# Kernel tuning notes

Hardware: AMD Instinct MI355X
Metric: run time of the kernel (lower is better)

The kernel has to match this reference:

```python
import jax, jax.numpy as jnp
import numpy as np

C = 256          # channels
H = 8            # attn_heads
B = 2048         # number of graphs
NPG = 128        # nodes per graph
N = B * NPG      # total nodes
EPS = 1e-5


def setup_inputs() -> dict:
    key = jax.random.key(0)
    ks = jax.random.split(key, 16)
    s = 1.0 / np.sqrt(C)
    seg = jnp.repeat(jnp.arange(B, dtype=jnp.int32), NPG)          # sorted, all segments present
    batch = jnp.stack([seg, seg], axis=1)                           # [N, 2]; column 0 = graph id
    return {
        "x": jax.random.normal(ks[0], (N, C), dtype=jnp.float32),
        "batch": batch,
        "num_graphs": B,
        "W1": jax.random.normal(ks[1], (C, C), dtype=jnp.float32) * s,
        "b1": jnp.zeros((C,), jnp.float32),
        "gamma": jnp.ones((C,), jnp.float32),
        "beta": jnp.zeros((C,), jnp.float32),
        "W2": jax.random.normal(ks[2], (C, C), dtype=jnp.float32) * s,
        "b2": jnp.zeros((C,), jnp.float32),
        "Wq": jax.random.normal(ks[3], (C, C), dtype=jnp.float32) * s,
        "bq": jnp.zeros((C,), jnp.float32),
        "Wk": jax.random.normal(ks[4], (C, C), dtype=jnp.float32) * s,
        "bk": jnp.zeros((C,), jnp.float32),
        "Wv": jax.random.normal(ks[5], (C, C), dtype=jnp.float32) * s,
        "bv": jnp.zeros((C,), jnp.float32),
        "Wo": jax.random.normal(ks[6], (C, C), dtype=jnp.float32) * s,
        "bo": jnp.zeros((C,), jnp.float32),
        "Wr": jax.random.normal(ks[7], (1, C), dtype=jnp.float32) * s,
        "br": jnp.zeros((1,), jnp.float32),
    }


def reference(x, batch, num_graphs, W1, b1, gamma, beta, W2, b2,
              Wq, bq, Wk, bk, Wv, bv, Wo, bo, Wr, br):
    seg = batch[:, 0]                                   # [N] graph ids, sorted
    Dh = C // H
    scale = 1.0 / np.sqrt(Dh)

    # trunk: Linear -> BatchNorm1d (train-mode batch stats) -> ReLU -> Linear
    h = x @ W1.T + b1                                   # [N, C]
    mu = h.mean(axis=0)
    var = h.var(axis=0)                                 # biased, as torch uses for normalization
    h = (h - mu) * jax.lax.rsqrt(var + EPS) * gamma + beta
    h = jax.nn.relu(h)
    h = h @ W2.T + b2                                   # [N, C]

    # single-query MHA pooled per graph segment (query = ones(C))
    q = jnp.ones((C,), h.dtype)
    qh = (q @ Wq.T + bq).reshape(H, Dh)                 # [H, Dh] shared across graphs
    kh = (h @ Wk.T + bk).reshape(N, H, Dh)              # [N, H, Dh]
    vh = (h @ Wv.T + bv).reshape(N, H, Dh)

    logits = jnp.einsum('nhd,hd->nh', kh, qh) * scale   # [N, H]
    # segment softmax over each graph's nodes
    m = jax.ops.segment_max(logits, seg, num_segments=num_graphs)   # [B, H]
    p = jnp.exp(logits - m[seg])                                     # [N, H]
    denom = jax.ops.segment_sum(p, seg, num_segments=num_graphs)     # [B, H]
    attn = p / denom[seg]                                            # [N, H]

    pooled = jax.ops.segment_sum(attn[:, :, None] * vh, seg,
                                 num_segments=num_graphs)            # [B, H, Dh]
    pooled = pooled.reshape(num_graphs, C) @ Wo.T + bo               # out_proj -> [B, C]

    out = jnp.tanh(pooled @ Wr.T + br)                               # [B, 1]
    return out
```

## Files before the change

### kernel.cpp

```cpp
#include <hip/hip_runtime.h>
#include <hip/hip_bf16.h>
#include <math.h>

#define C_DIM 256
#define H_HEADS 8
#define B_GRAPHS 2048
#define NPG 128
#define N_NODES (B_GRAPHS * NPG)
#define EPS 1e-5f
#define SCALE_ATT 0.17677669529663687f

typedef short bf16x8 __attribute__((ext_vector_type(8)));
typedef float f32x4 __attribute__((ext_vector_type(4)));

__device__ __forceinline__ unsigned short f2bf(float f) {
    __hip_bfloat16 h = __float2bfloat16(f);
    union { __hip_bfloat16 h; unsigned short u; } cv; cv.h = h; return cv.u;
}
__device__ __forceinline__ float bf2f(unsigned short u) {
    union { unsigned int i; float f; } v; v.i = ((unsigned int)u) << 16; return v.f;
}


__global__ __launch_bounds__(256) void prep1_kernel(
    const float* __restrict__ Wq, const float* __restrict__ bq,
    const float* __restrict__ Wk, const float* __restrict__ bk,
    const float* __restrict__ Wo, const float* __restrict__ Wr,
    float* __restrict__ wk_eff, float* __restrict__ lbias, float* __restrict__ wor)
{
    __shared__ float qhS[256];
    __shared__ float WrS[256];
    const int t = threadIdx.x;
    {
        float s = bq[t];
        const float* row = Wq + (size_t)t * 256;
        for (int c = 0; c < 256; c += 4) {
            float4 v = *(const float4*)&row[c];
            s += v.x + v.y + v.z + v.w;
        }
        qhS[t] = s;
        WrS[t] = Wr[t];
    }
    __syncthreads();
    for (int it = 0; it < 8; ++it) {
        int idx = t + it * 256;
        int head = idx >> 8, c = idx & 255;
        float acc = 0.f;
        #pragma unroll 4
        for (int d = 0; d < 32; ++d)
            acc = fmaf(Wk[(size_t)(head * 32 + d) * 256 + c], qhS[head * 32 + d], acc);
        wk_eff[head * 256 + c] = acc * SCALE_ATT;
    }
    if (t < 8) {
        float acc = 0.f;
        for (int d = 0; d < 32; ++d) acc = fmaf(bk[t * 32 + d], qhS[t * 32 + d], acc);
        lbias[t] = acc * SCALE_ATT;
    }
    {
        float acc = 0.f;
        for (int j2 = 0; j2 < 256; ++j2)
            acc = fmaf(Wo[(size_t)j2 * 256 + t], WrS[j2], acc);
        wor[t] = acc;
    }
}

__global__ __launch_bounds__(256) void prep2_kernel(
    const float* __restrict__ W2, const float* __restrict__ b2,
    const float* __restrict__ Wv, const float* __restrict__ wk_eff,
    const float* __restrict__ lbias, const float* __restrict__ wor_g,
    float* __restrict__ wfT, float* __restrict__ bfold, float* __restrict__ V_g)
{
    __shared__ float wkS[256];
    const int t = threadIdx.x, head = blockIdx.x;
    wkS[t] = wk_eff[head * 256 + t];
    __syncthreads();
    float acc = 0.f;
    #pragma unroll 4
    for (int cp = 0; cp < 256; ++cp)
        acc = fmaf(W2[(size_t)cp * 256 + t], wkS[cp], acc);
    wfT[head * 256 + t] = acc;
    float accv = 0.f;
    #pragma unroll 4
    for (int d = 0; d < 32; ++d) {
        int j = head * 32 + d;
        accv = fmaf(Wv[(size_t)j * 256 + t], wor_g[j], accv);
    }
    V_g[head * 256 + t] = accv;
    if (t == 0) {
        float b = lbias[head];
        for (int cp = 0; cp < 256; ++cp) b = fmaf(b2[cp], wkS[cp], b);
        bfold[head] = b;
    }
}

__global__ __launch_bounds__(256) void prep3_kernel(
    const float* __restrict__ W2, const float* __restrict__ V_g, float* __restrict__ G_g)
{
    __shared__ float vS[256];
    const int t = threadIdx.x, head = blockIdx.x;
    vS[t] = V_g[head * 256 + t];
    __syncthreads();
    float acc = 0.f;
    #pragma unroll 4
    for (int cp = 0; cp < 256; ++cp)
        acc = fmaf(W2[(size_t)cp * 256 + t], vS[cp], acc);
    G_g[t * 8 + head] = acc;
}

__global__ __launch_bounds__(256) void prep4_kernel(
    const float* __restrict__ b2, const float* __restrict__ bv,
    const float* __restrict__ bo, const float* __restrict__ Wr,
    const float* __restrict__ br, const float* __restrict__ V_g,
    const float* __restrict__ wor, float* __restrict__ c0)
{
    __shared__ float red[256];
    const int t = threadIdx.x;
    float vs = 0.f;
    #pragma unroll
    for (int h = 0; h < 8; ++h) vs += V_g[h * 256 + t];
    red[t] = b2[t] * vs + bv[t] * wor[t] + bo[t] * Wr[t];
    __syncthreads();
    for (int s = 128; s > 0; s >>= 1) {
        if (t < s) red[t] += red[t + s];
        __syncthreads();
    }
    if (t == 0) c0[0] = red[0] + br[0];
}

__global__ __launch_bounds__(256) void w1cvt_kernel(
    const float* __restrict__ W1, unsigned short* __restrict__ W1bf)
{
    int i = blockIdx.x * 256 + threadIdx.x;
    W1bf[i] = f2bf(W1[i]);
}

__global__ __launch_bounds__(256) void gemm1_kernel(
    const float* __restrict__ x, const unsigned short* __restrict__ W1bf,
    unsigned short* __restrict__ h1bf,
    float* __restrict__ parts1, float* __restrict__ parts2)
{
    __shared__ unsigned short Alds[128 * 40];
    __shared__ unsigned short Blds[256 * 40];
    const int t = threadIdx.x;
    const int lane = t & 63, w = t >> 6;
    const int l15 = lane & 15, kg = lane >> 4;
    const size_t n0 = (size_t)blockIdx.x * 128;

    f32x4 acc[2][16];
    #pragma unroll
    for (int mt = 0; mt < 2; ++mt)
        #pragma unroll
        for (int nt = 0; nt < 16; ++nt)
            acc[mt][nt] = (f32x4){0.f, 0.f, 0.f, 0.f};

    for (int kk = 0; kk < 8; ++kk) {
        if (kk) __syncthreads();
        #pragma unroll
        for (int p = 0; p < 4; ++p) {
            int i = p * 256 + t;
            {
                int row = i >> 3, kq = i & 7;
                float4 v = *(const float4*)&x[(n0 + row) * 256 + kk * 32 + kq * 4];
                ushort4 u;
                u.x = f2bf(v.x); u.y = f2bf(v.y); u.z = f2bf(v.z); u.w = f2bf(v.w);
                *(ushort4*)&Alds[row * 40 + kq * 4] = u;
            }
            {
                int row = i >> 2, seg = i & 3;
                bf16x8 bv = *(const bf16x8*)&W1bf[(size_t)row * 256 + kk * 32 + seg * 8];
                *(bf16x8*)&Blds[row * 40 + seg * 8] = bv;
            }
        }
        __syncthreads();
        bf16x8 a0 = *(const bf16x8*)&Alds[(w * 32 + l15) * 40 + kg * 8];
        bf16x8 a1 = *(const bf16x8*)&Alds[(w * 32 + 16 + l15) * 40 + kg * 8];
        #pragma unroll
        for (int nt = 0; nt < 16; ++nt) {
            bf16x8 b = *(const bf16x8*)&Blds[(nt * 16 + l15) * 40 + kg * 8];
            acc[0][nt] = __builtin_amdgcn_mfma_f32_16x16x32_bf16(a0, b, acc[0][nt], 0, 0, 0);
            acc[1][nt] = __builtin_amdgcn_mfma_f32_16x16x32_bf16(a1, b, acc[1][nt], 0, 0, 0);
        }
    }

    float s1[16], s2[16];
    #pragma unroll
    for (int nt = 0; nt < 16; ++nt) { s1[nt] = 0.f; s2[nt] = 0.f; }
    #pragma unroll
    for (int mt = 0; mt < 2; ++mt)
        #pragma unroll
        for (int nt = 0; nt < 16; ++nt)
            #pragma unroll
            for (int r = 0; r < 4; ++r) {
                float f = acc[mt][nt][r];
                size_t row = n0 + w * 32 + mt * 16 + kg * 4 + r;
                h1bf[row * 256 + nt * 16 + l15] = f2bf(f);
                s1[nt] += f;
                s2[nt] += f * f;
            }
    #pragma unroll
    for (int nt = 0; nt < 16; ++nt) {
        s1[nt] += __shfl_xor(s1[nt], 16);
        s1[nt] += __shfl_xor(s1[nt], 32);
        s2[nt] += __shfl_xor(s2[nt], 16);
        s2[nt] += __shfl_xor(s2[nt], 32);
    }
    if (lane < 16) {
        size_t prow = ((size_t)blockIdx.x * 4 + w) * 256;
        #pragma unroll
        for (int nt = 0; nt < 16; ++nt) {
            parts1[prow + nt * 16 + lane] = s1[nt];
            parts2[prow + nt * 16 + lane] = s2[nt];
        }
    }
}

__global__ __launch_bounds__(256) void reduce_kernel(
    const float* __restrict__ P1, const float* __restrict__ P2,
    float* __restrict__ psum, float* __restrict__ psum2)
{
    const int t = threadIdx.x;
    const int b = blockIdx.x;
    float s = 0.f, s2 = 0.f;
    for (int r = 0; r < 128; ++r) {
        size_t row = (size_t)(b * 128 + r) * 256;
        s += P1[row + t];
        s2 += P2[row + t];
    }
    atomicAdd(&psum[t], s);
    atomicAdd(&psum2[t], s2);
}

__global__ __launch_bounds__(256) void stats_kernel(
    const float* __restrict__ psum, const float* __restrict__ psum2,
    const float* __restrict__ gamma, const float* __restrict__ beta,
    float* __restrict__ sc, float* __restrict__ sh)
{
    const int t = threadIdx.x;
    const float invN = 1.0f / (float)N_NODES;
    float S = psum[t], S2 = psum2[t];
    float mu = S * invN;
    float var = S2 * invN - mu * mu;
    float rstd = rsqrtf(var + EPS);
    float g = gamma[t] * rstd;
    sc[t] = g;
    sh[t] = beta[t] - mu * g;
}

__global__ __launch_bounds__(256, 2) void fused_kernel(
    const unsigned short* __restrict__ h1bf, const float* __restrict__ sc_g,
    const float* __restrict__ sh_g, const float* __restrict__ wfT_g,
    const float* __restrict__ bfold, const float* __restrict__ G_g,
    const float* __restrict__ c0_g, float* __restrict__ out)
{
    __shared__ __align__(16) float S[13220];
    float* scS     = S;
    float* shS     = S + 256;
    float* wfTS    = S + 512;
    float* logitsS = S + 2560;
    float* attnS   = S + 3616;
    float* AtS     = S + 4640;
    float* redP    = S + 6688;
    float* redS    = S + 8992;
    unsigned short* aSu = (unsigned short*)(S + 8996);

    const int t = threadIdx.x;
    const int g = blockIdx.x;

    scS[t] = sc_g[t];
    shS[t] = sh_g[t];
    #pragma unroll
    for (int q = 0; q < 8; ++q) wfTS[t + q * 256] = wfT_g[t + q * 256];

    const int n_dot = t & 31, ce = t >> 5;
    const int h_red = t >> 5, n_red = t & 31;

    for (int chunk = 0; chunk < 4; ++chunk) {
        __syncthreads();
        #pragma unroll
        for (int p = 0; p < 4; ++p) {
            int i = p * 256 + t;
            int row = i >> 5, seg = i & 31;
            const bf16x8 hv = *(const bf16x8*)&h1bf[((size_t)(g * 128 + chunk * 32 + row)) * 256 + seg * 8];
            float4 sc0 = *(const float4*)&scS[seg * 8];
            float4 sc1 = *(const float4*)&scS[seg * 8 + 4];
            float4 sh0 = *(const float4*)&shS[seg * 8];
            float4 sh1 = *(const float4*)&shS[seg * 8 + 4];
            bf16x8 av;
            av[0] = (short)f2bf(fmaxf(fmaf(bf2f((unsigned short)hv[0]), sc0.x, sh0.x), 0.f));
            av[1] = (short)f2bf(fmaxf(fmaf(bf2f((unsigned short)hv[1]), sc0.y, sh0.y), 0.f));
            av[2] = (short)f2bf(fmaxf(fmaf(bf2f((unsigned short)hv[2]), sc0.z, sh0.z), 0.f));
            av[3] = (short)f2bf(fmaxf(fmaf(bf2f((unsigned short)hv[3]), sc0.w, sh0.w), 0.f));
            av[4] = (short)f2bf(fmaxf(fmaf(bf2f((unsigned short)hv[4]), sc1.x, sh1.x), 0.f));
            av[5] = (short)f2bf(fmaxf(fmaf(bf2f((unsigned short)hv[5]), sc1.y, sh1.y), 0.f));
            av[6] = (short)f2bf(fmaxf(fmaf(bf2f((unsigned short)hv[6]), sc1.z, sh1.z), 0.f));
            av[7] = (short)f2bf(fmaxf(fmaf(bf2f((unsigned short)hv[7]), sc1.w, sh1.w), 0.f));
            *(bf16x8*)&aSu[row * 264 + seg * 8] = av;
        }
        __syncthreads();
        {
            float lacc[8];
            #pragma unroll
            for (int h = 0; h < 8; ++h) lacc[h] = 0.f;
            #pragma unroll
            for (int i = 0; i < 4; ++i) {
                const bf16x8 a8 = *(const bf16x8*)&aSu[n_dot * 264 + ce * 32 + i * 8];
                float af[8];
                #pragma unroll
                for (int j = 0; j < 8; ++j) af[j] = bf2f((unsigned short)a8[j]);
                #pragma unroll
                for (int h = 0; h < 8; ++h) {
                    const float4 w0 = *(const float4*)&wfTS[h * 256 + ce * 32 + i * 8];
                    const float4 w1 = *(const float4*)&wfTS[h * 256 + ce * 32 + i * 8 + 4];
                    lacc[h] = fmaf(af[0], w0.x, fmaf(af[1], w0.y, fmaf(af[2], w0.z, fmaf(af[3], w0.w,
                              fmaf(af[4], w1.x, fmaf(af[5], w1.y, fmaf(af[6], w1.z, fmaf(af[7], w1.w, lacc[h]))))))));
                }
            }
            #pragma unroll
            for (int h = 0; h < 8; ++h) redP[(ce * 32 + n_dot) * 9 + h] = lacc[h];
        }
        __syncthreads();
        {
            float L = bfold[h_red];
            #pragma unroll
            for (int ce2 = 0; ce2 < 8; ++ce2) L += redP[(ce2 * 32 + n_red) * 9 + h_red];
            logitsS[h_red * 132 + chunk * 32 + n_red] = L;
        }
    }
    __syncthreads();

    {
        const int head = t >> 5, j = t & 31;
        float l0 = logitsS[head * 132 + j];
        float l1 = logitsS[head * 132 + j + 32];
        float l2 = logitsS[head * 132 + j + 64];
        float l3 = logitsS[head * 132 + j + 96];
        float m = fmaxf(fmaxf(l0, l1), fmaxf(l2, l3));
        for (int s = 16; s > 0; s >>= 1) m = fmaxf(m, __shfl_xor(m, s, 32));
        float p0 = expf(l0 - m), p1 = expf(l1 - m), p2 = expf(l2 - m), p3 = expf(l3 - m);
        float sum = p0 + p1 + p2 + p3;
        for (int s = 16; s > 0; s >>= 1) sum += __shfl_xor(sum, s, 32);
        float inv = 1.0f / sum;
        attnS[(j + 0) * 8 + head] = p0 * inv;
        attnS[(j + 32) * 8 + head] = p1 * inv;
        attnS[(j + 64) * 8 + head] = p2 * inv;
        attnS[(j + 96) * 8 + head] = p3 * inv;
    }
    __syncthreads();

    {
        float acc[8];
        #pragma unroll
        for (int h = 0; h < 8; ++h) acc[h] = 0.f;
        const float scv = scS[t], shv = shS[t];
        const unsigned short* hp = h1bf + (size_t)g * 128 * 256 + t;
        #pragma unroll 4
        for (int n = 0; n < 128; ++n) {
            float hv = bf2f(hp[n * 256]);
            float a = fmaxf(fmaf(hv, scv, shv), 0.f);
            const float4 w0 = *(const float4*)&attnS[n * 8];
            const float4 w1 = *(const float4*)&attnS[n * 8 + 4];
            acc[0] = fmaf(a, w0.x, acc[0]);
            acc[1] = fmaf(a, w0.y, acc[1]);
            acc[2] = fmaf(a, w0.z, acc[2]);
            acc[3] = fmaf(a, w0.w, acc[3]);
            acc[4] = fmaf(a, w1.x, acc[4]);
            acc[5] = fmaf(a, w1.y, acc[5]);
            acc[6] = fmaf(a, w1.z, acc[6]);
            acc[7] = fmaf(a, w1.w, acc[7]);
        }
        #pragma unroll
        for (int h = 0; h < 8; ++h) AtS[t * 8 + h] = acc[h];
    }
    __syncthreads();

    {
        float4 a0 = *(const float4*)&AtS[t * 8];
        float4 a1 = *(const float4*)&AtS[t * 8 + 4];
        float4 g0 = *(const float4*)&G_g[t * 8];
        float4 g1 = *(const float4*)&G_g[t * 8 + 4];
        float term = a0.x * g0.x + a0.y * g0.y + a0.z * g0.z + a0.w * g0.w +
                     a1.x * g1.x + a1.y * g1.y + a1.z * g1.z + a1.w * g1.w;
        for (int s = 32; s > 0; s >>= 1) term += __shfl_xor(term, s);
        if ((t & 63) == 0) redS[t >> 6] = term;
        __syncthreads();
        if (t == 0) out[g] = tanhf(redS[0] + redS[1] + redS[2] + redS[3] + c0_g[0]);
    }
}

#define FOFF_WKE 0
#define FOFF_LB  2048
#define FOFF_WFT 2064
#define FOFF_BFD 4112
#define FOFF_WOR 4128
#define FOFF_V   4384
#define FOFF_G   6432
#define FOFF_C0  8480
#define FOFF_PS  8484
#define FOFF_PS2 8740
#define FOFF_SC  8996
#define FOFF_SH  9252
#define FOFF_P1  9512
#define FOFF_P2  (9512 + 2097152)

extern "C" void kernel_launch(void* const* d_in, const int* in_sizes, int n_in,
                              void* d_out, int out_size, void* d_ws, size_t ws_size,
                              hipStream_t stream)
{
    (void)in_sizes; (void)n_in; (void)out_size; (void)ws_size;
    const float* x     = (const float*)d_in[0];
    const float* W1    = (const float*)d_in[3];
    const float* gamma = (const float*)d_in[5];
    const float* beta  = (const float*)d_in[6];
    const float* W2    = (const float*)d_in[7];
    const float* b2    = (const float*)d_in[8];
    const float* Wq    = (const float*)d_in[9];
    const float* bq    = (const float*)d_in[10];
    const float* Wk    = (const float*)d_in[11];
    const float* bk    = (const float*)d_in[12];
    const float* Wv    = (const float*)d_in[13];
    const float* bv    = (const float*)d_in[14];
    const float* Wo    = (const float*)d_in[15];
    const float* bo    = (const float*)d_in[16];
    const float* Wr    = (const float*)d_in[17];
    const float* br    = (const float*)d_in[18];

    unsigned short* h1bf = (unsigned short*)d_ws;
    unsigned short* W1bf = h1bf + (size_t)N_NODES * 256;
    float* fbase = (float*)(W1bf + 65536);

    float* wk_eff = fbase + FOFF_WKE;
    float* lbias  = fbase + FOFF_LB;
    float* wfT    = fbase + FOFF_WFT;
    float* bfold  = fbase + FOFF_BFD;
    float* wor    = fbase + FOFF_WOR;
    float* V_g    = fbase + FOFF_V;
    float* G_g    = fbase + FOFF_G;
    float* c0     = fbase + FOFF_C0;
    float* psum   = fbase + FOFF_PS;
    float* psum2  = fbase + FOFF_PS2;
    float* sc     = fbase + FOFF_SC;
    float* sh     = fbase + FOFF_SH;
    float* P1     = fbase + FOFF_P1;
    float* P2     = fbase + FOFF_P2;

    hipMemsetAsync((void*)psum, 0, 512 * sizeof(float), stream);

    hipLaunchKernelGGL(prep1_kernel, dim3(1), dim3(256), 0, stream,
                       Wq, bq, Wk, bk, Wo, Wr, wk_eff, lbias, wor);
    hipLaunchKernelGGL(w1cvt_kernel, dim3(256), dim3(256), 0, stream, W1, W1bf);
    hipLaunchKernelGGL(prep2_kernel, dim3(8), dim3(256), 0, stream,
                       W2, b2, Wv, wk_eff, lbias, wor, wfT, bfold, V_g);
    hipLaunchKernelGGL(prep3_kernel, dim3(8), dim3(256), 0, stream, W2, V_g, G_g);
    hipLaunchKernelGGL(prep4_kernel, dim3(1), dim3(256), 0, stream,
                       b2, bv, bo, Wr, br, V_g, wor, c0);
    hipLaunchKernelGGL(gemm1_kernel, dim3(N_NODES / 128), dim3(256), 0, stream,
                       x, W1bf, h1bf, P1, P2);
    hipLaunchKernelGGL(reduce_kernel, dim3(64), dim3(256), 0, stream, P1, P2, psum, psum2);
    hipLaunchKernelGGL(stats_kernel, dim3(1), dim3(256), 0, stream,
                       psum, psum2, gamma, beta, sc, sh);
    hipLaunchKernelGGL(fused_kernel, dim3(B_GRAPHS), dim3(256), 0, stream,
                       h1bf, sc, sh, wfT, bfold, G_g, c0, (float*)d_out);
}
```

Measured before the change: 647.0 us.

## Compute per-graph logits and value projections with MFMA over a repacked h1 layout

```diff
diff --git a/kernel.cpp b/kernel.cpp
--- a/kernel.cpp
+++ b/kernel.cpp
@@ -9,6 +9,7 @@
 #define N_NODES (B_GRAPHS * NPG)
 #define EPS 1e-5f
 #define SCALE_ATT 0.17677669529663687f
+#define AST 264
 
 typedef short bf16x8 __attribute__((ext_vector_type(8)));
 typedef float f32x4 __attribute__((ext_vector_type(4)));
@@ -24,9 +25,9 @@
 
 __global__ __launch_bounds__(256) void prep1_kernel(
     const float* __restrict__ Wq, const float* __restrict__ bq,
-    const float* __restrict__ Wk, const float* __restrict__ bk,
+    const float* __restrict__ Wk,
     const float* __restrict__ Wo, const float* __restrict__ Wr,
-    float* __restrict__ wk_eff, float* __restrict__ lbias, float* __restrict__ wor)
+    float* __restrict__ wk_eff, float* __restrict__ wor)
 {
     __shared__ float qhS[256];
     __shared__ float WrS[256];
@@ -51,11 +52,6 @@
             acc = fmaf(Wk[(size_t)(head * 32 + d) * 256 + c], qhS[head * 32 + d], acc);
         wk_eff[head * 256 + c] = acc * SCALE_ATT;
     }
-    if (t < 8) {
-        float acc = 0.f;
-        for (int d = 0; d < 32; ++d) acc = fmaf(bk[t * 32 + d], qhS[t * 32 + d], acc);
-        lbias[t] = acc * SCALE_ATT;
-    }
     {
         float acc = 0.f;
         for (int j2 = 0; j2 < 256; ++j2)
@@ -65,10 +61,9 @@
 }
 
 __global__ __launch_bounds__(256) void prep2_kernel(
-    const float* __restrict__ W2, const float* __restrict__ b2,
-    const float* __restrict__ Wv, const float* __restrict__ wk_eff,
-    const float* __restrict__ lbias, const float* __restrict__ wor_g,
-    float* __restrict__ wfT, float* __restrict__ bfold, float* __restrict__ V_g)
+    const float* __restrict__ W2, const float* __restrict__ Wv,
+    const float* __restrict__ wk_eff, const float* __restrict__ wor_g,
+    unsigned short* __restrict__ WBg, float* __restrict__ V_g)
 {
     __shared__ float wkS[256];
     const int t = threadIdx.x, head = blockIdx.x;
@@ -78,7 +73,7 @@
     #pragma unroll 4
     for (int cp = 0; cp < 256; ++cp)
         acc = fmaf(W2[(size_t)cp * 256 + t], wkS[cp], acc);
-    wfT[head * 256 + t] = acc;
+    WBg[head * 256 + t] = f2bf(acc);
     float accv = 0.f;
     #pragma unroll 4
     for (int d = 0; d < 32; ++d) {
@@ -86,15 +81,11 @@
         accv = fmaf(Wv[(size_t)j * 256 + t], wor_g[j], accv);
     }
     V_g[head * 256 + t] = accv;
-    if (t == 0) {
-        float b = lbias[head];
-        for (int cp = 0; cp < 256; ++cp) b = fmaf(b2[cp], wkS[cp], b);
-        bfold[head] = b;
-    }
 }
 
 __global__ __launch_bounds__(256) void prep3_kernel(
-    const float* __restrict__ W2, const float* __restrict__ V_g, float* __restrict__ G_g)
+    const float* __restrict__ W2, const float* __restrict__ V_g,
+    unsigned short* __restrict__ WBg)
 {
     __shared__ float vS[256];
     const int t = threadIdx.x, head = blockIdx.x;
@@ -104,7 +95,7 @@
     #pragma unroll 4
     for (int cp = 0; cp < 256; ++cp)
         acc = fmaf(W2[(size_t)cp * 256 + t], vS[cp], acc);
-    G_g[t * 8 + head] = acc;
+    WBg[(8 + head) * 256 + t] = f2bf(acc);
 }
 
 __global__ __launch_bounds__(256) void prep4_kernel(
@@ -136,7 +127,7 @@
 
 __global__ __launch_bounds__(256) void gemm1_kernel(
     const float* __restrict__ x, const unsigned short* __restrict__ W1bf,
-    unsigned short* __restrict__ h1bf,
+    unsigned short* __restrict__ h1s,
     float* __restrict__ parts1, float* __restrict__ parts2)
 {
     __shared__ unsigned short Alds[128 * 40];
@@ -185,18 +176,19 @@
     float s1[16], s2[16];
     #pragma unroll
     for (int nt = 0; nt < 16; ++nt) { s1[nt] = 0.f; s2[nt] = 0.f; }
+    const size_t rowqBase = (n0 >> 2) + (size_t)w * 8;
     #pragma unroll
     for (int mt = 0; mt < 2; ++mt)
         #pragma unroll
-        for (int nt = 0; nt < 16; ++nt)
-            #pragma unroll
-            for (int r = 0; r < 4; ++r) {
-                float f = acc[mt][nt][r];
-                size_t row = n0 + w * 32 + mt * 16 + kg * 4 + r;
-                h1bf[row * 256 + nt * 16 + l15] = f2bf(f);
-                s1[nt] += f;
-                s2[nt] += f * f;
-            }
+        for (int nt = 0; nt < 16; ++nt) {
+            float f0 = acc[mt][nt][0], f1 = acc[mt][nt][1];
+            float f2v = acc[mt][nt][2], f3 = acc[mt][nt][3];
+            s1[nt] += (f0 + f1) + (f2v + f3);
+            s2[nt] += (f0 * f0 + f1 * f1) + (f2v * f2v + f3 * f3);
+            ushort4 u;
+            u.x = f2bf(f0); u.y = f2bf(f1); u.z = f2bf(f2v); u.w = f2bf(f3);
+            *(ushort4*)&h1s[(rowqBase + mt * 4 + kg) * 1024 + (nt * 16 + l15) * 4] = u;
+        }
     #pragma unroll
     for (int nt = 0; nt < 16; ++nt) {
         s1[nt] += __shfl_xor(s1[nt], 16);
@@ -246,161 +238,116 @@
     sh[t] = beta[t] - mu * g;
 }
 
-__global__ __launch_bounds__(256, 2) void fused_kernel(
-    const unsigned short* __restrict__ h1bf, const float* __restrict__ sc_g,
-    const float* __restrict__ sh_g, const float* __restrict__ wfT_g,
-    const float* __restrict__ bfold, const float* __restrict__ G_g,
+__global__ __launch_bounds__(256, 1) void fused_kernel(
+    const unsigned short* __restrict__ h1s, const float* __restrict__ sc_g,
+    const float* __restrict__ sh_g, const unsigned short* __restrict__ WBg,
     const float* __restrict__ c0_g, float* __restrict__ out)
 {
-    __shared__ __align__(16) float S[13220];
-    float* scS     = S;
-    float* shS     = S + 256;
-    float* wfTS    = S + 512;
-    float* logitsS = S + 2560;
-    float* attnS   = S + 3616;
-    float* AtS     = S + 4640;
-    float* redP    = S + 6688;
-    float* redS    = S + 8992;
-    unsigned short* aSu = (unsigned short*)(S + 8996);
+    __shared__ __align__(16) unsigned short aS[128 * AST];
+    __shared__ __align__(16) unsigned short WBl[16 * AST];
+    __shared__ float scS[256], shS[256];
+    __shared__ float LG[128 * 17];
+    __shared__ float redH[8];
+    __shared__ float c0S;
 
     const int t = threadIdx.x;
     const int g = blockIdx.x;
+    const int lane = t & 63, w = t >> 6;
+    const int l15 = lane & 15, kg = lane >> 4;
 
     scS[t] = sc_g[t];
     shS[t] = sh_g[t];
-    #pragma unroll
-    for (int q = 0; q < 8; ++q) wfTS[t + q * 256] = wfT_g[t + q * 256];
-
-    const int n_dot = t & 31, ce = t >> 5;
-    const int h_red = t >> 5, n_red = t & 31;
-
-    for (int chunk = 0; chunk < 4; ++chunk) {
-        __syncthreads();
-        #pragma unroll
-        for (int p = 0; p < 4; ++p) {
-            int i = p * 256 + t;
-            int row = i >> 5, seg = i & 31;
-            const bf16x8 hv = *(const bf16x8*)&h1bf[((size_t)(g * 128 + chunk * 32 + row)) * 256 + seg * 8];
-            float4 sc0 = *(const float4*)&scS[seg * 8];
-            float4 sc1 = *(const float4*)&scS[seg * 8 + 4];
-            float4 sh0 = *(const float4*)&shS[seg * 8];
-            float4 sh1 = *(const float4*)&shS[seg * 8 + 4];
-            bf16x8 av;
-            av[0] = (short)f2bf(fmaxf(fmaf(bf2f((unsigned short)hv[0]), sc0.x, sh0.x), 0.f));
-            av[1] = (short)f2bf(fmaxf(fmaf(bf2f((unsigned short)hv[1]), sc0.y, sh0.y), 0.f));
-            av[2] = (short)f2bf(fmaxf(fmaf(bf2f((unsigned short)hv[2]), sc0.z, sh0.z), 0.f));
-            av[3] = (short)f2bf(fmaxf(fmaf(bf2f((unsigned short)hv[3]), sc0.w, sh0.w), 0.f));
-            av[4] = (short)f2bf(fmaxf(fmaf(bf2f((unsigned short)hv[4]), sc1.x, sh1.x), 0.f));
-            av[5] = (short)f2bf(fmaxf(fmaf(bf2f((unsigned short)hv[5]), sc1.y, sh1.y), 0.f));
-            av[6] = (short)f2bf(fmaxf(fmaf(bf2f((unsigned short)hv[6]), sc1.z, sh1.z), 0.f));
-            av[7] = (short)f2bf(fmaxf(fmaf(bf2f((unsigned short)hv[7]), sc1.w, sh1.w), 0.f));
-            *(bf16x8*)&aSu[row * 264 + seg * 8] = av;
-        }
-        __syncthreads();
-        {
-            float lacc[8];
-            #pragma unroll
-            for (int h = 0; h < 8; ++h) lacc[h] = 0.f;
-            #pragma unroll
-            for (int i = 0; i < 4; ++i) {
-                const bf16x8 a8 = *(const bf16x8*)&aSu[n_dot * 264 + ce * 32 + i * 8];
-                float af[8];
-                #pragma unroll
-                for (int j = 0; j < 8; ++j) af[j] = bf2f((unsigned short)a8[j]);
-                #pragma unroll
-                for (int h = 0; h < 8; ++h) {
-                    const float4 w0 = *(const float4*)&wfTS[h * 256 + ce * 32 + i * 8];
-                    const float4 w1 = *(const float4*)&wfTS[h * 256 + ce * 32 + i * 8 + 4];
-                    lacc[h] = fmaf(af[0], w0.x, fmaf(af[1], w0.y, fmaf(af[2], w0.z, fmaf(af[3], w0.w,
-                              fmaf(af[4], w1.x, fmaf(af[5], w1.y, fmaf(af[6], w1.z, fmaf(af[7], w1.w, lacc[h]))))))));
-                }
-            }
-            #pragma unroll
-            for (int h = 0; h < 8; ++h) redP[(ce * 32 + n_dot) * 9 + h] = lacc[h];
-        }
-        __syncthreads();
-        {
-            float L = bfold[h_red];
-            #pragma unroll
-            for (int ce2 = 0; ce2 < 8; ++ce2) L += redP[(ce2 * 32 + n_red) * 9 + h_red];
-            logitsS[h_red * 132 + chunk * 32 + n_red] = L;
-        }
-    }
-    __syncthreads();
-
     {
-        const int head = t >> 5, j = t & 31;
-        float l0 = logitsS[head * 132 + j];
-        float l1 = logitsS[head * 132 + j + 32];
-        float l2 = logitsS[head * 132 + j + 64];
-        float l3 = logitsS[head * 132 + j + 96];
-        float m = fmaxf(fmaxf(l0, l1), fmaxf(l2, l3));
+        int j = t >> 4, cc = (t & 15) * 16;
+        bf16x8 w0 = *(const bf16x8*)&WBg[j * 256 + cc];
+        bf16x8 w1 = *(const bf16x8*)&WBg[j * 256 + cc + 8];
+        *(bf16x8*)&WBl[j * AST + cc] = w0;
+        *(bf16x8*)&WBl[j * AST + cc + 8] = w1;
+    }
+    if (t == 0) c0S = c0_g[0];
+    __syncthreads();
+
+    const unsigned short* hg = h1s + (size_t)g * 32768;
+    unsigned int* aS32 = (unsigned int*)aS;
+    #pragma unroll 4
+    for (int it = 0; it < 16; ++it) {
+        int i = it * 256 + t;
+        int rowq = i >> 7, cp = i & 127, cc0 = cp * 2;
+        bf16x8 hv = *(const bf16x8*)&hg[rowq * 1024 + cp * 8];
+        float sc0 = scS[cc0], sc1 = scS[cc0 + 1];
+        float sh0 = shS[cc0], sh1 = shS[cc0 + 1];
+        #pragma unroll
+        for (int r = 0; r < 4; ++r) {
+            float a0 = fmaxf(fmaf(bf2f((unsigned short)hv[r]), sc0, sh0), 0.f);
+            float a1 = fmaxf(fmaf(bf2f((unsigned short)hv[r + 4]), sc1, sh1), 0.f);
+            unsigned int pk = (unsigned int)f2bf(a0) | ((unsigned int)f2bf(a1) << 16);
+            aS32[((rowq * 4 + r) * AST + cc0) >> 1] = pk;
+        }
+    }
+    __syncthreads();
+
+    {
+        const int m0 = w * 32;
+        f32x4 acc0 = {0.f, 0.f, 0.f, 0.f}, acc1 = {0.f, 0.f, 0.f, 0.f};
+        #pragma unroll
+        for (int kt = 0; kt < 8; ++kt) {
+            bf16x8 b  = *(const bf16x8*)&WBl[l15 * AST + kt * 32 + kg * 8];
+            bf16x8 a0 = *(const bf16x8*)&aS[(m0 + l15) * AST + kt * 32 + kg * 8];
+            bf16x8 a1 = *(const bf16x8*)&aS[(m0 + 16 + l15) * AST + kt * 32 + kg * 8];
+            acc0 = __builtin_amdgcn_mfma_f32_16x16x32_bf16(a0, b, acc0, 0, 0, 0);
+            acc1 = __builtin_amdgcn_mfma_f32_16x16x32_bf16(a1, b, acc1, 0, 0, 0);
+        }
+        #pragma unroll
+        for (int r = 0; r < 4; ++r) {
+            LG[(m0 + kg * 4 + r) * 17 + l15] = acc0[r];
+            LG[(m0 + 16 + kg * 4 + r) * 17 + l15] = acc1[r];
+        }
+    }
+    __syncthreads();
+
+    {
+        const int h = t >> 5, j = t & 31;
+        float l[4], gv[4];
+        #pragma unroll
+        for (int q = 0; q < 4; ++q) {
+            int n = j + q * 32;
+            l[q]  = LG[n * 17 + h];
+            gv[q] = LG[n * 17 + 8 + h];
+        }
+        float m = fmaxf(fmaxf(l[0], l[1]), fmaxf(l[2], l[3]));
         for (int s = 16; s > 0; s >>= 1) m = fmaxf(m, __shfl_xor(m, s, 32));
-        float p0 = expf(l0 - m), p1 = expf(l1 - m), p2 = expf(l2 - m), p3 = expf(l3 - m);
-        float sum = p0 + p1 + p2 + p3;
-        for (int s = 16; s > 0; s >>= 1) sum += __shfl_xor(sum, s, 32);
-        float inv = 1.0f / sum;
-        attnS[(j + 0) * 8 + head] = p0 * inv;
-        attnS[(j + 32) * 8 + head] = p1 * inv;
-        attnS[(j + 64) * 8 + head] = p2 * inv;
-        attnS[(j + 96) * 8 + head] = p3 * inv;
-    }
-    __syncthreads();
-
-    {
-        float acc[8];
-        #pragma unroll
-        for (int h = 0; h < 8; ++h) acc[h] = 0.f;
-        const float scv = scS[t], shv = shS[t];
-        const unsigned short* hp = h1bf + (size_t)g * 128 * 256 + t;
-        #pragma unroll 4
-        for (int n = 0; n < 128; ++n) {
-            float hv = bf2f(hp[n * 256]);
-            float a = fmaxf(fmaf(hv, scv, shv), 0.f);
-            const float4 w0 = *(const float4*)&attnS[n * 8];
-            const float4 w1 = *(const float4*)&attnS[n * 8 + 4];
-            acc[0] = fmaf(a, w0.x, acc[0]);
-            acc[1] = fmaf(a, w0.y, acc[1]);
-            acc[2] = fmaf(a, w0.z, acc[2]);
-            acc[3] = fmaf(a, w0.w, acc[3]);
-            acc[4] = fmaf(a, w1.x, acc[4]);
-            acc[5] = fmaf(a, w1.y, acc[5]);
-            acc[6] = fmaf(a, w1.z, acc[6]);
-            acc[7] = fmaf(a, w1.w, acc[7]);
-        }
-        #pragma unroll
-        for (int h = 0; h < 8; ++h) AtS[t * 8 + h] = acc[h];
-    }
-    __syncthreads();
-
-    {
-        float4 a0 = *(const float4*)&AtS[t * 8];
-        float4 a1 = *(const float4*)&AtS[t * 8 + 4];
-        float4 g0 = *(const float4*)&G_g[t * 8];
-        float4 g1 = *(const float4*)&G_g[t * 8 + 4];
-        float term = a0.x * g0.x + a0.y * g0.y + a0.z * g0.z + a0.w * g0.w +
-                     a1.x * g1.x + a1.y * g1.y + a1.z * g1.z + a1.w * g1.w;
-        for (int s = 32; s > 0; s >>= 1) term += __shfl_xor(term, s);
-        if ((t & 63) == 0) redS[t >> 6] = term;
-        __syncthreads();
-        if (t == 0) out[g] = tanhf(redS[0] + redS[1] + redS[2] + redS[3] + c0_g[0]);
+        float sp = 0.f, sg = 0.f;
+        #pragma unroll
+        for (int q = 0; q < 4; ++q) {
+            float p = expf(l[q] - m);
+            sp += p;
+            sg = fmaf(p, gv[q], sg);
+        }
+        for (int s = 16; s > 0; s >>= 1) {
+            sp += __shfl_xor(sp, s, 32);
+            sg += __shfl_xor(sg, s, 32);
+        }
+        if (j == 0) redH[h] = sg / sp;
+    }
+    __syncthreads();
+    if (t == 0) {
+        float r = c0S;
+        #pragma unroll
+        for (int h = 0; h < 8; ++h) r += redH[h];
+        out[g] = tanhf(r);
     }
 }
 
 #define FOFF_WKE 0
-#define FOFF_LB  2048
-#define FOFF_WFT 2064
-#define FOFF_BFD 4112
-#define FOFF_WOR 4128
-#define FOFF_V   4384
-#define FOFF_G   6432
-#define FOFF_C0  8480
-#define FOFF_PS  8484
-#define FOFF_PS2 8740
-#define FOFF_SC  8996
-#define FOFF_SH  9252
-#define FOFF_P1  9512
-#define FOFF_P2  (9512 + 2097152)
+#define FOFF_WOR 2048
+#define FOFF_V   2304
+#define FOFF_C0  4352
+#define FOFF_PS  4368
+#define FOFF_PS2 4624
+#define FOFF_SC  4880
+#define FOFF_SH  5136
+#define FOFF_P1  5392
+#define FOFF_P2  (5392 + 2097152)
 
 extern "C" void kernel_launch(void* const* d_in, const int* in_sizes, int n_in,
                               void* d_out, int out_size, void* d_ws, size_t ws_size,
@@ -416,7 +363,6 @@
     const float* Wq    = (const float*)d_in[9];
     const float* bq    = (const float*)d_in[10];
     const float* Wk    = (const float*)d_in[11];
-    const float* bk    = (const float*)d_in[12];
     const float* Wv    = (const float*)d_in[13];
     const float* bv    = (const float*)d_in[14];
     const float* Wo    = (const float*)d_in[15];
@@ -424,17 +370,14 @@
     const float* Wr    = (const float*)d_in[17];
     const float* br    = (const float*)d_in[18];
 
-    unsigned short* h1bf = (unsigned short*)d_ws;
-    unsigned short* W1bf = h1bf + (size_t)N_NODES * 256;
-    float* fbase = (float*)(W1bf + 65536);
+    unsigned short* h1s  = (unsigned short*)d_ws;
+    unsigned short* W1bf = h1s + (size_t)N_NODES * 256;
+    unsigned short* WBg  = W1bf + 65536;
+    float* fbase = (float*)(WBg + 4096);
 
     float* wk_eff = fbase + FOFF_WKE;
-    float* lbias  = fbase + FOFF_LB;
-    float* wfT    = fbase + FOFF_WFT;
-    float* bfold  = fbase + FOFF_BFD;
     float* wor    = fbase + FOFF_WOR;
     float* V_g    = fbase + FOFF_V;
-    float* G_g    = fbase + FOFF_G;
     float* c0     = fbase + FOFF_C0;
     float* psum   = fbase + FOFF_PS;
     float* psum2  = fbase + FOFF_PS2;
@@ -446,18 +389,18 @@
     hipMemsetAsync((void*)psum, 0, 512 * sizeof(float), stream);
 
     hipLaunchKernelGGL(prep1_kernel, dim3(1), dim3(256), 0, stream,
-                       Wq, bq, Wk, bk, Wo, Wr, wk_eff, lbias, wor);
+                       Wq, bq, Wk, Wo, Wr, wk_eff, wor);
     hipLaunchKernelGGL(w1cvt_kernel, dim3(256), dim3(256), 0, stream, W1, W1bf);
     hipLaunchKernelGGL(prep2_kernel, dim3(8), dim3(256), 0, stream,
-                       W2, b2, Wv, wk_eff, lbias, wor, wfT, bfold, V_g);
-    hipLaunchKernelGGL(prep3_kernel, dim3(8), dim3(256), 0, stream, W2, V_g, G_g);
+                       W2, Wv, wk_eff, wor, WBg, V_g);
+    hipLaunchKernelGGL(prep3_kernel, dim3(8), dim3(256), 0, stream, W2, V_g, WBg);
     hipLaunchKernelGGL(prep4_kernel, dim3(1), dim3(256), 0, stream,
                        b2, bv, bo, Wr, br, V_g, wor, c0);
     hipLaunchKernelGGL(gemm1_kernel, dim3(N_NODES / 128), dim3(256), 0, stream,
-                       x, W1bf, h1bf, P1, P2);
+                       x, W1bf, h1s, P1, P2);
     hipLaunchKernelGGL(reduce_kernel, dim3(64), dim3(256), 0, stream, P1, P2, psum, psum2);
     hipLaunchKernelGGL(stats_kernel, dim3(1), dim3(256), 0, stream,
                        psum, psum2, gamma, beta, sc, sh);
     hipLaunchKernelGGL(fused_kernel, dim3(B_GRAPHS), dim3(256), 0, stream,
-                       h1bf, sc, sh, wfT, bfold, G_g, c0, (float*)d_out);
-}
+                       h1s, sc, sh, WBg, c0, (float*)d_out);
+}
```

New measurement: 588.2 us. 9.1% less time.
